# Optimization experiments

Hardware: AMD Instinct MI355X
Metric: run time of the kernel (lower is better)

Reference implementation:

```python
import jax, jax.numpy as jnp
import numpy as np

B, V, D = 8, 1024, 512
H = 8
HD = D // H
MAX_HOP = 8


def setup_inputs() -> dict:
    key = jax.random.key(0)
    ks = jax.random.split(key, 5)
    x = jax.random.normal(ks[0], (B, V, D), dtype=jnp.float32)
    w_qkv = jax.random.normal(ks[1], (D, 3 * D), dtype=jnp.float32) * (D ** -0.5)
    w_out = jax.random.normal(ks[2], (D, D), dtype=jnp.float32) * (D ** -0.5)
    b_out = jnp.zeros((D,), dtype=jnp.float32)
    rpe_bias = jax.random.normal(ks[3], (H, MAX_HOP + 1), dtype=jnp.float32) * 0.02
    hop_matrix = jax.random.randint(ks[4], (V, V), 0, MAX_HOP + 1, dtype=jnp.int32)
    return {"x": x, "w_qkv": w_qkv, "w_out": w_out, "b_out": b_out,
            "rpe_bias": rpe_bias, "hop_matrix": hop_matrix}


def reference(x, w_qkv, w_out, b_out, rpe_bias, hop_matrix):
    b, v, d = x.shape
    scale = HD ** -0.5
    qkv = x @ w_qkv                                   # [B, V, 3D]
    q, k, val = jnp.split(qkv, 3, axis=-1)
    # [B, V, D] -> [B, H, V, HD]
    def split_heads(t):
        return t.reshape(b, v, H, HD).transpose(0, 2, 1, 3)
    q, k, val = split_heads(q), split_heads(k), split_heads(val)
    scores = jnp.einsum('bhvd,bhwd->bhvw', q, k)      # [B, H, V, V]
    bias = rpe_bias[:, hop_matrix]                    # gather -> [H, V, V]
    attn = jax.nn.softmax((scores + bias[None]) * scale, axis=-1)
    out_heads = jnp.einsum('bhvw,bhwd->bhvd', attn, val)
    out = out_heads.transpose(0, 2, 1, 3).reshape(b, v, d)
    out = out @ w_out + b_out
    return out, attn
```

## Files before the change

kernel.cpp:

```cpp
#include <hip/hip_runtime.h>

typedef __attribute__((ext_vector_type(8))) short bf16x8;
typedef __attribute__((ext_vector_type(4))) float f32x4;

#define MFMA16(A,B,C) __builtin_amdgcn_mfma_f32_16x16x32_bf16(A,B,C,0,0,0)

__device__ __forceinline__ unsigned short f2bf(float f){
  unsigned int u = __float_as_uint(f);
  u += 0x7FFFu + ((u >> 16) & 1u);
  return (unsigned short)(u >> 16);
}
__device__ __forceinline__ float bf2f(unsigned short s){
  return __uint_as_float(((unsigned int)s) << 16);
}
__device__ __forceinline__ int swz(int row, int kbyte){
  return (row * 128 + kbyte) ^ ((row & 7) << 4);
}

__global__ __launch_bounds__(256) void k_prep(
    const float* __restrict__ w_qkv, const float* __restrict__ w_out,
    unsigned short* __restrict__ wqT, unsigned short* __restrict__ woT)
{
  int idx = blockIdx.x * 256 + threadIdx.x;
  if (idx < 1536 * 512) {
    int n = idx >> 9, kq = idx & 511;
    wqT[idx] = f2bf(w_qkv[(size_t)kq * 1536 + n]);
  } else {
    int j = idx - 1536 * 512;
    int n = j >> 9, kq = j & 511;
    woT[j] = f2bf(w_out[(size_t)kq * 512 + n]);
  }
}

__global__ __launch_bounds__(256) void k_bias(
    const int* __restrict__ hop, const float* __restrict__ rpe_bias,
    unsigned short* __restrict__ biasT)
{
  __shared__ float rl[72];
  const int tid = threadIdx.x;
  if (tid < 72) rl[tid] = rpe_bias[tid];
  __syncthreads();
  const int idx = blockIdx.x * 256 + tid;
  const int hv = hop[idx];
#pragma unroll
  for (int h = 0; h < 8; ++h)
    biasT[((size_t)h << 20) + idx] = f2bf(rl[h * 9 + hv]);
}

__global__ __launch_bounds__(256) void k_qkv(
    const float* __restrict__ x, const unsigned short* __restrict__ wqT,
    unsigned short* __restrict__ q, unsigned short* __restrict__ k_,
    unsigned short* __restrict__ valT)
{
  __shared__ char lds[32768];
  char* At = lds; char* Bt = lds + 16384;
  const int tid = threadIdx.x;
  const int wid = tid >> 6, lane = tid & 63, g = lane >> 4, r = lane & 15;
  const int wm = wid >> 1, wn = wid & 1;
  const int m0 = blockIdx.x * 128, n0 = blockIdx.y * 128;

  f32x4 acc[4][4];
#pragma unroll
  for (int a = 0; a < 4; ++a)
#pragma unroll
    for (int b = 0; b < 4; ++b) acc[a][b] = (f32x4){0.f, 0.f, 0.f, 0.f};

  for (int kt = 0; kt < 8; ++kt) {
    const int k0 = kt * 64;
    __syncthreads();
#pragma unroll
    for (int it = 0; it < 8; ++it) {
      int c = tid + it * 256;
      int row = c >> 4, c4 = c & 15;
      float4 xv = *reinterpret_cast<const float4*>(x + (size_t)(m0 + row) * 512 + k0 + c4 * 4);
      uint2 hv;
      hv.x = (unsigned)f2bf(xv.x) | ((unsigned)f2bf(xv.y) << 16);
      hv.y = (unsigned)f2bf(xv.z) | ((unsigned)f2bf(xv.w) << 16);
      *reinterpret_cast<uint2*>(At + swz(row, c4 * 8)) = hv;
    }
#pragma unroll
    for (int it = 0; it < 4; ++it) {
      int c = tid + it * 256;
      int row = c >> 3, c8 = c & 7;
      *reinterpret_cast<uint4*>(Bt + swz(row, c8 * 16)) =
          *reinterpret_cast<const uint4*>(wqT + (size_t)(n0 + row) * 512 + k0 + c8 * 8);
    }
    __syncthreads();
#pragma unroll
    for (int kk = 0; kk < 2; ++kk) {
      bf16x8 af[4], bf[4];
      const int kb = (kk * 32 + 8 * g) * 2;
#pragma unroll
      for (int mi = 0; mi < 4; ++mi)
        af[mi] = *reinterpret_cast<const bf16x8*>(At + swz(wm * 64 + mi * 16 + r, kb));
#pragma unroll
      for (int ni = 0; ni < 4; ++ni)
        bf[ni] = *reinterpret_cast<const bf16x8*>(Bt + swz(wn * 64 + ni * 16 + r, kb));
#pragma unroll
      for (int mi = 0; mi < 4; ++mi)
#pragma unroll
        for (int ni = 0; ni < 4; ++ni)
          acc[mi][ni] = MFMA16(af[mi], bf[ni], acc[mi][ni]);
    }
  }
  const int s = n0 >> 9;
#pragma unroll
  for (int mi = 0; mi < 4; ++mi)
#pragma unroll
    for (int ni = 0; ni < 4; ++ni)
#pragma unroll
      for (int i = 0; i < 4; ++i) {
        int m = m0 + wm * 64 + mi * 16 + 4 * g + i;
        int n = n0 + wn * 64 + ni * 16 + r;
        int b = m >> 10, v = m & 1023;
        int cc = n & 511, h = cc >> 6, d = cc & 63;
        int bh = b * 8 + h;
        unsigned short bfv = f2bf(acc[mi][ni][i]);
        if (s == 2)      valT[((size_t)bh * 64 + d) * 1024 + v] = bfv;
        else if (s == 0) q [((size_t)bh * 1024 + v) * 64 + d] = bfv;
        else             k_[((size_t)bh * 1024 + v) * 64 + d] = bfv;
      }
}

__global__ __launch_bounds__(256, 3) void k_attn(
    const unsigned short* __restrict__ q, const unsigned short* __restrict__ k_,
    const unsigned short* __restrict__ valT,
    const unsigned short* __restrict__ biasT,
    float* __restrict__ attn, unsigned short* __restrict__ oh)
{
  __shared__ unsigned short P[16 * 1040];
  __shared__ float red[2][4][16];
  const int tid = threadIdx.x;
  const int wid = tid >> 6, lane = tid & 63, g = lane >> 4, r = lane & 15;
  const int blk = blockIdx.x;
  const int vt = blk & 63, bh = blk >> 6, h = bh & 7;
  const int v0 = vt * 16;

  const unsigned short* bb = biasT + ((size_t)h << 20) + (size_t)v0 * 1024;
#pragma unroll
  for (int it = 0; it < 8; ++it) {
    int e = tid + it * 256;
    int row = e >> 7, c8 = e & 127;
    *reinterpret_cast<uint4*>(&P[row * 1040 + c8 * 8]) =
        *reinterpret_cast<const uint4*>(bb + (size_t)row * 1024 + c8 * 8);
  }

  const unsigned short* qp = q + ((size_t)bh * 1024 + v0) * 64;
  bf16x8 qf[2];
#pragma unroll
  for (int kk = 0; kk < 2; ++kk)
    qf[kk] = *reinterpret_cast<const bf16x8*>(qp + r * 64 + kk * 32 + 8 * g);
  __syncthreads();

  const unsigned short* kb = k_ + (size_t)bh * 65536;
  f32x4 s[16];
#pragma unroll
  for (int ct = 0; ct < 16; ++ct) {
    const int wcol = wid * 256 + ct * 16 + r;
    f32x4 acc = (f32x4){0.f, 0.f, 0.f, 0.f};
#pragma unroll
    for (int kk = 0; kk < 2; ++kk) {
      bf16x8 kf = *reinterpret_cast<const bf16x8*>(kb + (size_t)wcol * 64 + kk * 32 + 8 * g);
      acc = MFMA16(qf[kk], kf, acc);
    }
#pragma unroll
    for (int i = 0; i < 4; ++i)
      s[ct][i] = (acc[i] + bf2f(P[(4 * g + i) * 1040 + wcol])) * 0.125f;
  }

  float mx[4] = {-1e30f, -1e30f, -1e30f, -1e30f};
#pragma unroll
  for (int ct = 0; ct < 16; ++ct)
#pragma unroll
    for (int i = 0; i < 4; ++i) mx[i] = fmaxf(mx[i], s[ct][i]);
#pragma unroll
  for (int o = 1; o <= 8; o <<= 1)
#pragma unroll
    for (int i = 0; i < 4; ++i) mx[i] = fmaxf(mx[i], __shfl_xor(mx[i], o, 64));
  if (r == 0)
#pragma unroll
    for (int i = 0; i < 4; ++i) red[0][wid][4 * g + i] = mx[i];
  __syncthreads();
#pragma unroll
  for (int i = 0; i < 4; ++i) {
    float M = red[0][0][4 * g + i];
#pragma unroll
    for (int w = 1; w < 4; ++w) M = fmaxf(M, red[0][w][4 * g + i]);
    mx[i] = M;
  }

  float sm[4] = {0.f, 0.f, 0.f, 0.f};
#pragma unroll
  for (int ct = 0; ct < 16; ++ct)
#pragma unroll
    for (int i = 0; i < 4; ++i) {
      float e = __expf(s[ct][i] - mx[i]);
      s[ct][i] = e;
      sm[i] += e;
    }
#pragma unroll
  for (int o = 1; o <= 8; o <<= 1)
#pragma unroll
    for (int i = 0; i < 4; ++i) sm[i] += __shfl_xor(sm[i], o, 64);
  if (r == 0)
#pragma unroll
    for (int i = 0; i < 4; ++i) red[1][wid][4 * g + i] = sm[i];
  __syncthreads();
  float inv[4];
#pragma unroll
  for (int i = 0; i < 4; ++i) {
    float T = red[1][0][4 * g + i] + red[1][1][4 * g + i] +
              red[1][2][4 * g + i] + red[1][3][4 * g + i];
    inv[i] = 1.0f / T;
  }

  float* ab = attn + ((size_t)bh * 1024 + v0) * 1024;
#pragma unroll
  for (int ct = 0; ct < 16; ++ct) {
    const int col = wid * 256 + ct * 16 + r;
#pragma unroll
    for (int i = 0; i < 4; ++i) {
      const int row = 4 * g + i;
      float a = s[ct][i] * inv[i];
      __builtin_nontemporal_store(a, ab + (size_t)row * 1024 + col);
      P[row * 1040 + col] = f2bf(a);
    }
  }
  __syncthreads();

  const unsigned short* vT = valT + ((size_t)bh * 64 + wid * 16) * 1024;
  f32x4 acc = (f32x4){0.f, 0.f, 0.f, 0.f};
  for (int kc = 0; kc < 32; ++kc) {
    bf16x8 pa = *reinterpret_cast<const bf16x8*>(&P[r * 1040 + kc * 32 + 8 * g]);
    bf16x8 vb = *reinterpret_cast<const bf16x8*>(vT + (size_t)r * 1024 + kc * 32 + 8 * g);
    acc = MFMA16(pa, vb, acc);
  }
  const int b = bh >> 3;
#pragma unroll
  for (int i = 0; i < 4; ++i) {
    size_t oi = ((size_t)(b * 1024 + v0 + 4 * g + i)) * 512 + h * 64 + wid * 16 + r;
    oh[oi] = f2bf(acc[i]);
  }
}

__global__ __launch_bounds__(256) void k_out(
    const unsigned short* __restrict__ oh, const unsigned short* __restrict__ woT,
    const float* __restrict__ b_out, float* __restrict__ out)
{
  __shared__ char lds[32768];
  char* At = lds; char* Bt = lds + 16384;
  const int tid = threadIdx.x;
  const int wid = tid >> 6, lane = tid & 63, g = lane >> 4, r = lane & 15;
  const int wm = wid >> 1, wn = wid & 1;
  const int m0 = blockIdx.x * 128, n0 = blockIdx.y * 128;

  f32x4 acc[4][4];
#pragma unroll
  for (int a = 0; a < 4; ++a)
#pragma unroll
    for (int b = 0; b < 4; ++b) acc[a][b] = (f32x4){0.f, 0.f, 0.f, 0.f};

  for (int kt = 0; kt < 8; ++kt) {
    const int k0 = kt * 64;
    __syncthreads();
#pragma unroll
    for (int it = 0; it < 4; ++it) {
      int c = tid + it * 256;
      int row = c >> 3, c8 = c & 7;
      *reinterpret_cast<uint4*>(At + swz(row, c8 * 16)) =
          *reinterpret_cast<const uint4*>(oh + (size_t)(m0 + row) * 512 + k0 + c8 * 8);
      *reinterpret_cast<uint4*>(Bt + swz(row, c8 * 16)) =
          *reinterpret_cast<const uint4*>(woT + (size_t)(n0 + row) * 512 + k0 + c8 * 8);
    }
    __syncthreads();
#pragma unroll
    for (int kk = 0; kk < 2; ++kk) {
      bf16x8 a4[4], b4[4];
      const int kb = (kk * 32 + 8 * g) * 2;
#pragma unroll
      for (int mi = 0; mi < 4; ++mi)
        a4[mi] = *reinterpret_cast<const bf16x8*>(At + swz(wm * 64 + mi * 16 + r, kb));
#pragma unroll
      for (int ni = 0; ni < 4; ++ni)
        b4[ni] = *reinterpret_cast<const bf16x8*>(Bt + swz(wn * 64 + ni * 16 + r, kb));
#pragma unroll
      for (int mi = 0; mi < 4; ++mi)
#pragma unroll
        for (int ni = 0; ni < 4; ++ni)
          acc[mi][ni] = MFMA16(a4[mi], b4[ni], acc[mi][ni]);
    }
  }
#pragma unroll
  for (int mi = 0; mi < 4; ++mi)
#pragma unroll
    for (int ni = 0; ni < 4; ++ni)
#pragma unroll
      for (int i = 0; i < 4; ++i) {
        int m = m0 + wm * 64 + mi * 16 + 4 * g + i;
        int n = n0 + wn * 64 + ni * 16 + r;
        __builtin_nontemporal_store(acc[mi][ni][i] + b_out[n], out + (size_t)m * 512 + n);
      }
}

extern "C" void kernel_launch(void* const* d_in, const int* in_sizes, int n_in,
                              void* d_out, int out_size, void* d_ws, size_t ws_size,
                              hipStream_t stream) {
  const float *x = nullptr, *w_qkv = nullptr, *w_out = nullptr,
              *b_out = nullptr, *rpe = nullptr;
  const int* hop = nullptr;
  for (int i = 0; i < n_in; ++i) {
    switch (in_sizes[i]) {
      case 4194304: x     = (const float*)d_in[i]; break;
      case 786432:  w_qkv = (const float*)d_in[i]; break;
      case 262144:  w_out = (const float*)d_in[i]; break;
      case 512:     b_out = (const float*)d_in[i]; break;
      case 72:      rpe   = (const float*)d_in[i]; break;
      case 1048576: hop   = (const int*)d_in[i];   break;
    }
  }

  float* out  = (float*)d_out;
  float* attn = out + (size_t)4194304;

  char* ws = (char*)d_ws;
  unsigned short* q_    = (unsigned short*)(ws);
  unsigned short* k_    = (unsigned short*)(ws + (size_t) 8388608);
  unsigned short* valT  = (unsigned short*)(ws + (size_t)16777216);
  unsigned short* oh    = (unsigned short*)(ws + (size_t)25165824);
  unsigned short* wqT   = (unsigned short*)(ws + (size_t)33554432);
  unsigned short* woT   = (unsigned short*)(ws + (size_t)35127296);
  unsigned short* biasT = (unsigned short*)(ws + (size_t)35651584);

  k_prep<<<dim3(4096), dim3(256), 0, stream>>>(w_qkv, w_out, wqT, woT);
  k_bias<<<dim3(4096), dim3(256), 0, stream>>>(hop, rpe, biasT);
  k_qkv<<<dim3(64, 12), dim3(256), 0, stream>>>(x, wqT, q_, k_, valT);
  k_attn<<<dim3(4096), dim3(256), 0, stream>>>(q_, k_, valT, biasT, attn, oh);
  k_out<<<dim3(64, 4), dim3(256), 0, stream>>>(oh, woT, b_out, out);
}
```

Measured before the change: 209.7 us.

## Stage attention probabilities in LDS and write them out as coalesced vector stores

The attention kernel now writes normalized probabilities only to LDS as bf16 and then streams them to global memory with 16-byte coalesced nontemporal stores, instead of scattered 4-byte stores from the MFMA layout. The LDS row stride changes from 1040 to 1032, and the P@V loop is split into two independent accumulators to expose more MFMA parallelism. The returned attention matrix is now rounded through bf16, which lowers its precision relative to the fp32 values written before.

```diff
diff --git a/kernel.cpp b/kernel.cpp
--- a/kernel.cpp
+++ b/kernel.cpp
@@ -122,13 +122,14 @@
       }
 }
 
+#define PSTR 1032
 __global__ __launch_bounds__(256, 3) void k_attn(
     const unsigned short* __restrict__ q, const unsigned short* __restrict__ k_,
     const unsigned short* __restrict__ valT,
     const unsigned short* __restrict__ biasT,
     float* __restrict__ attn, unsigned short* __restrict__ oh)
 {
-  __shared__ unsigned short P[16 * 1040];
+  __shared__ unsigned short P[16 * PSTR];
   __shared__ float red[2][4][16];
   const int tid = threadIdx.x;
   const int wid = tid >> 6, lane = tid & 63, g = lane >> 4, r = lane & 15;
@@ -141,7 +142,7 @@
   for (int it = 0; it < 8; ++it) {
     int e = tid + it * 256;
     int row = e >> 7, c8 = e & 127;
-    *reinterpret_cast<uint4*>(&P[row * 1040 + c8 * 8]) =
+    *reinterpret_cast<uint4*>(&P[row * PSTR + c8 * 8]) =
         *reinterpret_cast<const uint4*>(bb + (size_t)row * 1024 + c8 * 8);
   }
 
@@ -165,7 +166,7 @@
     }
 #pragma unroll
     for (int i = 0; i < 4; ++i)
-      s[ct][i] = (acc[i] + bf2f(P[(4 * g + i) * 1040 + wcol])) * 0.125f;
+      s[ct][i] = (acc[i] + bf2f(P[(4 * g + i) * PSTR + wcol])) * 0.125f;
   }
 
   float mx[4] = {-1e30f, -1e30f, -1e30f, -1e30f};
@@ -214,27 +215,41 @@
     inv[i] = 1.0f / T;
   }
 
-  float* ab = attn + ((size_t)bh * 1024 + v0) * 1024;
 #pragma unroll
   for (int ct = 0; ct < 16; ++ct) {
     const int col = wid * 256 + ct * 16 + r;
 #pragma unroll
-    for (int i = 0; i < 4; ++i) {
-      const int row = 4 * g + i;
-      float a = s[ct][i] * inv[i];
-      __builtin_nontemporal_store(a, ab + (size_t)row * 1024 + col);
-      P[row * 1040 + col] = f2bf(a);
-    }
-  }
-  __syncthreads();
+    for (int i = 0; i < 4; ++i)
+      P[(4 * g + i) * PSTR + col] = f2bf(s[ct][i] * inv[i]);
+  }
+  __syncthreads();
+
+  float* ab = attn + ((size_t)bh * 1024 + v0) * 1024;
+#pragma unroll
+  for (int it = 0; it < 16; ++it) {
+    int e = tid + it * 256;
+    int row = e >> 8, q4 = e & 255;
+    uint2 pv = *reinterpret_cast<const uint2*>(&P[row * PSTR + q4 * 4]);
+    f32x4 o;
+    o[0] = bf2f((unsigned short)(pv.x      ));
+    o[1] = bf2f((unsigned short)(pv.x >> 16));
+    o[2] = bf2f((unsigned short)(pv.y      ));
+    o[3] = bf2f((unsigned short)(pv.y >> 16));
+    __builtin_nontemporal_store(o, reinterpret_cast<f32x4*>(ab + (size_t)row * 1024 + q4 * 4));
+  }
 
   const unsigned short* vT = valT + ((size_t)bh * 64 + wid * 16) * 1024;
-  f32x4 acc = (f32x4){0.f, 0.f, 0.f, 0.f};
-  for (int kc = 0; kc < 32; ++kc) {
-    bf16x8 pa = *reinterpret_cast<const bf16x8*>(&P[r * 1040 + kc * 32 + 8 * g]);
-    bf16x8 vb = *reinterpret_cast<const bf16x8*>(vT + (size_t)r * 1024 + kc * 32 + 8 * g);
-    acc = MFMA16(pa, vb, acc);
-  }
+  f32x4 a0 = (f32x4){0.f,0.f,0.f,0.f}, a1 = a0;
+  for (int kc = 0; kc < 32; kc += 2) {
+    const int base = r * PSTR, vbase = kc * 32 + 8 * g;
+    bf16x8 p0 = *reinterpret_cast<const bf16x8*>(&P[base + vbase]);
+    bf16x8 p1 = *reinterpret_cast<const bf16x8*>(&P[base + vbase + 32]);
+    bf16x8 v0_ = *reinterpret_cast<const bf16x8*>(vT + (size_t)r * 1024 + vbase);
+    bf16x8 v1_ = *reinterpret_cast<const bf16x8*>(vT + (size_t)r * 1024 + vbase + 32);
+    a0 = MFMA16(p0, v0_, a0);
+    a1 = MFMA16(p1, v1_, a1);
+  }
+  f32x4 acc = a0 + a1;
   const int b = bh >> 3;
 #pragma unroll
   for (int i = 0; i < 4; ++i) {
@@ -298,7 +313,8 @@
       for (int i = 0; i < 4; ++i) {
         int m = m0 + wm * 64 + mi * 16 + 4 * g + i;
         int n = n0 + wn * 64 + ni * 16 + r;
-        __builtin_nontemporal_store(acc[mi][ni][i] + b_out[n], out + (size_t)m * 512 + n);
+        float v = acc[mi][ni][i] + b_out[n];
+        __builtin_nontemporal_store(v, out + (size_t)m * 512 + n);
       }
 }
 
```

Result: faster. 205.1 us (-2.2%).
